# Performance work log

Measured on AMD Instinct MI355X. Metric: run time of the kernel, lower is better.

## Reference

```python
import jax, jax.numpy as jnp
import numpy as np

B, N, D, H, DG = 1, 1024, 512, 8, 64
DK = D // H
EPS = 1e-5


def _layer_norm(x, g, b):
    m = jnp.mean(x, axis=-1, keepdims=True)
    v = jnp.var(x, axis=-1, keepdims=True)
    return (x - m) / jnp.sqrt(v + EPS) * g + b


def _box_rel_embedding(box):
    # box: (B, N, 4) = x_min, y_min, x_max, y_max
    x_min, y_min, x_max, y_max = [box[..., i] for i in range(4)]  # each (B, N)
    cx = (x_min + x_max) * 0.5
    cy = (y_min + y_max) * 0.5
    w = x_max - x_min + 1.0
    h = y_max - y_min + 1.0
    dx = jnp.log(jnp.clip(jnp.abs((cx[:, :, None] - cx[:, None, :]) / w[:, :, None]), 0.001))
    dy = jnp.log(jnp.clip(jnp.abs((cy[:, :, None] - cy[:, None, :]) / h[:, :, None]), 0.001))
    dw = jnp.log(w[:, :, None] / w[:, None, :])
    dh = jnp.log(h[:, :, None] / h[:, None, :])
    pos = jnp.stack([dx, dy, dw, dh], axis=-1)  # (B, N, N, 4)
    dim_mat = 1.0 / jnp.power(1000.0, jnp.arange(DG // 8, dtype=jnp.float32) / (DG // 8))  # (8,)
    mul = (100.0 * pos[..., None] * dim_mat).reshape(pos.shape[0], pos.shape[1], pos.shape[2], -1)  # (B,N,N,32)
    return jnp.concatenate([jnp.sin(mul), jnp.cos(mul)], axis=-1)  # (B, N, N, 64)


def _split_heads(x, W, b):
    # torch permute(2,0,1,3).view(-1, len, d_k): head-major flattening
    return (x @ W.T + b).reshape(B, N, H, DK).transpose(2, 0, 1, 3).reshape(H * B, N, DK)


def _forward(input_query, input_key, input_value, input_box,
             Wq, bq, Wk, bk, Wv, bv, Wo, bo, WG_w, WG_b,
             ln0_g, ln0_b, ln_g, ln_b):
    residual = input_query
    emb = _box_rel_embedding(input_box)  # (B, N, N, 64)
    # per-head linear (64 -> 1) then relu: (B, H, N, N)
    w_g = jax.nn.relu(jnp.einsum('bijg,hg->bhij', emb, WG_w) + WG_b[None, :, None, None])
    q = _split_heads(input_query, Wq, bq)  # (H*B, N, DK)
    k = _split_heads(input_key, Wk, bk)
    v = _split_heads(input_value, Wv, bv)
    scores = jnp.einsum('xnd,xmd->xnm', q, k) / np.sqrt(DK).astype(np.float32)  # (H*B, N, N)
    # original adds (B,H,N,N) to (H*B,N,N): only valid for B==1
    w_mn = jax.nn.softmax(jnp.log(jnp.clip(w_g.reshape(H * B, N, N), 1e-6)) + scores, axis=-1)
    x = jnp.einsum('xnm,xmd->xnd', w_mn, v)  # (H*B, N, DK)
    # faithful to original: transpose(1,2) then view(nbatches, -1, h*d_k)
    x = x.transpose(0, 2, 1).reshape(B, -1, H * DK)  # (B, N, D)
    out0 = _layer_norm(x + residual, ln0_g, ln0_b)
    out = out0 @ Wo.T + bo  # dropout = identity (eval mode)
    return _layer_norm(out + out0, ln_g, ln_b)


def setup_inputs() -> dict:
    key = jax.random.key(0)
    ks = jax.random.split(key, 12)
    inp = {}
    inp['input_query'] = jax.random.normal(ks[0], (B, N, D), dtype=jnp.float32)
    inp['input_key'] = jax.random.normal(ks[1], (B, N, D), dtype=jnp.float32)
    inp['input_value'] = jax.random.normal(ks[2], (B, N, D), dtype=jnp.float32)
    mins = jax.random.uniform(ks[3], (B, N, 2), dtype=jnp.float32) * 500.0
    sizes = jax.random.uniform(ks[4], (B, N, 2), dtype=jnp.float32) * 99.0 + 1.0
    inp['input_box'] = jnp.concatenate([mins, mins + sizes], axis=-1)  # valid boxes
    s = 0.02
    inp['Wq'] = jax.random.normal(ks[5], (D, D), dtype=jnp.float32) * s
    inp['bq'] = jnp.zeros((D,), dtype=jnp.float32)
    inp['Wk'] = jax.random.normal(ks[6], (D, D), dtype=jnp.float32) * s
    inp['bk'] = jnp.zeros((D,), dtype=jnp.float32)
    inp['Wv'] = jax.random.normal(ks[7], (D, D), dtype=jnp.float32) * s
    inp['bv'] = jnp.zeros((D,), dtype=jnp.float32)
    inp['Wo'] = jax.random.normal(ks[8], (D, D), dtype=jnp.float32) * s
    inp['bo'] = jnp.zeros((D,), dtype=jnp.float32)
    inp['WG_w'] = jax.random.normal(ks[9], (H, DG), dtype=jnp.float32) * 0.1
    inp['WG_b'] = jax.random.normal(ks[10], (H,), dtype=jnp.float32) * 0.1
    inp['ln0_g'] = jnp.ones((D,), dtype=jnp.float32)
    inp['ln0_b'] = jnp.zeros((D,), dtype=jnp.float32)
    inp['ln_g'] = jnp.ones((D,), dtype=jnp.float32)
    inp['ln_b'] = jnp.zeros((D,), dtype=jnp.float32)
    return inp


def reference(input_query, input_key, input_value, input_box,
              Wq, bq, Wk, bk, Wv, bv, Wo, bo, WG_w, WG_b,
              ln0_g, ln0_b, ln_g, ln_b):
    return _forward(input_query, input_key, input_value, input_box,
                    Wq, bq, Wk, bk, Wv, bv, Wo, bo, WG_w, WG_b,
                    ln0_g, ln0_b, ln_g, ln_b)
```

## Files before the change

kernel.cpp:

```cpp
#include <hip/hip_runtime.h>
#include <cstddef>

#define NTOK 1024
#define DMODEL 512
#define NHEAD 8
#define DKH 64
#define NSPLIT 8
#define JQ 128

typedef __attribute__((ext_vector_type(4))) float f32x4;
typedef __attribute__((ext_vector_type(8))) __bf16 bf16x8;
typedef __attribute__((ext_vector_type(4))) __bf16 bf16x4;
typedef __attribute__((ext_vector_type(4))) unsigned short u16x4;
typedef __attribute__((ext_vector_type(8))) unsigned short u16x8;
typedef __attribute__((ext_vector_type(4))) _Float16 f16x4;
typedef unsigned short ushort_t;

__device__ __forceinline__ float wave_sum_f(float v){
  #pragma unroll
  for (int m=1; m<64; m<<=1) v += __shfl_xor(v, m, 64);
  return v;
}
__device__ __forceinline__ unsigned short f2bf(float f){
  __bf16 b = (__bf16)f;
  return __builtin_bit_cast(unsigned short, b);
}
__device__ __forceinline__ float bf2f(unsigned short u){
  return (float)__builtin_bit_cast(__bf16, u);
}

__device__ __forceinline__ float fract_hw(float x){
  float r; asm("v_fract_f32 %0, %1" : "=v"(r) : "v"(x)); return r;
}
__device__ __forceinline__ float sin_rev(float rev){
  float f = fract_hw(rev);
  float s; asm("v_sin_f32 %0, %1" : "=v"(s) : "v"(f)); return s;
}
__device__ __forceinline__ float cos_rev(float rev){
  float f = fract_hw(rev);
  float c; asm("v_cos_f32 %0, %1" : "=v"(c) : "v"(f)); return c;
}
__device__ __forceinline__ float log_hw(float x){
  float l; asm("v_log_f32 %0, %1" : "=v"(l) : "v"(x));
  return 0.69314718056f * l;
}
__device__ __forceinline__ float exp_hw(float x){
  float y = x * 1.44269504f;
  float e; asm("v_exp_f32 %0, %1" : "=v"(e) : "v"(y));
  return e;
}

__global__ __launch_bounds__(256) void k_front2(
    const float* __restrict__ box, const float* __restrict__ WGw, const float* __restrict__ WGb,
    _Float16* __restrict__ wg16,
    const float* __restrict__ inq, const float* __restrict__ ink, const float* __restrict__ inv,
    const float* __restrict__ Wq, const float* __restrict__ Wk, const float* __restrict__ Wv,
    const float* __restrict__ Wo,
    const float* __restrict__ bq, const float* __restrict__ bk, const float* __restrict__ bv,
    ushort_t* __restrict__ Qb, ushort_t* __restrict__ Kb, ushort_t* __restrict__ Vt,
    ushort_t* __restrict__ Wob){
  __shared__ __align__(16) char smem[17408];
  const int t = threadIdx.x;
  const int lane = t & 63, w = t >> 6, li = lane & 15, g = lane >> 4;
  if (blockIdx.x >= 1408){
    int off = ((blockIdx.x - 1408)*256 + t)*8;
    float4 a = *(const float4*)(Wo + off);
    float4 b4 = *(const float4*)(Wo + off + 4);
    u16x4 o0, o1;
    o0[0]=f2bf(a.x); o0[1]=f2bf(a.y); o0[2]=f2bf(a.z); o0[3]=f2bf(a.w);
    o1[0]=f2bf(b4.x); o1[1]=f2bf(b4.y); o1[2]=f2bf(b4.z); o1[3]=f2bf(b4.w);
    *(u16x4*)(Wob + off) = o0;
    *(u16x4*)(Wob + off + 4) = o1;
    return;
  }
  if (blockIdx.x >= 1024){
    const int u = blockIdx.x - 1024;
    const int z = u >> 7;
    const int rem = u & 127;
    const int m0 = (rem >> 3)*64;
    const int n0 = (rem & 7)*64;
    const float* A = z==0 ? inq : z==1 ? ink : inv;
    const float* W = z==0 ? Wq : z==1 ? Wk : Wv;
    const float* bias = z==0 ? bq : z==1 ? bk : bv;
    ushort_t* Al = (ushort_t*)smem;
    ushort_t* Wl = (ushort_t*)(smem + 8704);
    const int row = t >> 2, kq = (t & 3)*16;
    const int mrb = (w >> 1)*32;
    const int nrb = (w & 1)*32;
    f32x4 acc[2][2] = {};
    for (int k0 = 0; k0 < DMODEL; k0 += 64){
      {
        const float* ap = A + (size_t)(m0+row)*DMODEL + k0 + kq;
        const float* wp = W + (size_t)(n0+row)*DMODEL + k0 + kq;
        #pragma unroll
        for (int q=0; q<4; q++){
          float4 av = *(const float4*)(ap + q*4);
          float4 wv = *(const float4*)(wp + q*4);
          u16x4 pa, pw;
          pa[0]=f2bf(av.x); pa[1]=f2bf(av.y); pa[2]=f2bf(av.z); pa[3]=f2bf(av.w);
          pw[0]=f2bf(wv.x); pw[1]=f2bf(wv.y); pw[2]=f2bf(wv.z); pw[3]=f2bf(wv.w);
          *(u16x4*)(Al + row*68 + kq + q*4) = pa;
          *(u16x4*)(Wl + row*68 + kq + q*4) = pw;
        }
      }
      __syncthreads();
      #pragma unroll
      for (int kc=0; kc<64; kc+=32){
        const ushort_t* arl = Al + (mrb + li)*68 + kc + g*8;
        const ushort_t* wrl = Wl + (nrb + li)*68 + kc + g*8;
        bf16x8 af0 = *(const bf16x8*)(arl);
        bf16x8 af1 = *(const bf16x8*)(arl + 16*68);
        bf16x8 wf0 = *(const bf16x8*)(wrl);
        bf16x8 wf1 = *(const bf16x8*)(wrl + 16*68);
        if (z < 2){
          acc[0][0] = __builtin_amdgcn_mfma_f32_16x16x32_bf16(wf0, af0, acc[0][0], 0,0,0);
          acc[0][1] = __builtin_amdgcn_mfma_f32_16x16x32_bf16(wf0, af1, acc[0][1], 0,0,0);
          acc[1][0] = __builtin_amdgcn_mfma_f32_16x16x32_bf16(wf1, af0, acc[1][0], 0,0,0);
          acc[1][1] = __builtin_amdgcn_mfma_f32_16x16x32_bf16(wf1, af1, acc[1][1], 0,0,0);
        } else {
          acc[0][0] = __builtin_amdgcn_mfma_f32_16x16x32_bf16(af0, wf0, acc[0][0], 0,0,0);
          acc[0][1] = __builtin_amdgcn_mfma_f32_16x16x32_bf16(af0, wf1, acc[0][1], 0,0,0);
          acc[1][0] = __builtin_amdgcn_mfma_f32_16x16x32_bf16(af1, wf0, acc[1][0], 0,0,0);
          acc[1][1] = __builtin_amdgcn_mfma_f32_16x16x32_bf16(af1, wf1, acc[1][1], 0,0,0);
        }
      }
      __syncthreads();
    }
    if (z < 2){
      ushort_t* C = z ? Kb : Qb;
      #pragma unroll
      for (int nf=0; nf<2; nf++){
        int n = n0 + nrb + nf*16 + g*4;
        float4 b4 = *(const float4*)(bias + n);
        const float* bp = (const float*)&b4;
        #pragma unroll
        for (int mf=0; mf<2; mf++){
          int m = m0 + mrb + mf*16 + li;
          u16x4 o;
          #pragma unroll
          for (int r=0; r<4; r++) o[r] = f2bf(acc[nf][mf][r] + bp[r]);
          *(u16x4*)(C + (size_t)m*DMODEL + n) = o;
        }
      }
    } else {
      #pragma unroll
      for (int mf=0; mf<2; mf++){
        int m = m0 + mrb + mf*16 + g*4;
        #pragma unroll
        for (int nf=0; nf<2; nf++){
          int n = n0 + nrb + nf*16 + li;
          float bn = bias[n];
          u16x4 o;
          #pragma unroll
          for (int r=0; r<4; r++) o[r] = f2bf(acc[mf][nf][r] + bn);
          *(u16x4*)(Vt + (((size_t)(n>>6))<<16) + ((size_t)(n&63)<<10) + m) = o;
        }
      }
    }
    return;
  }
  float* arr = (float*)smem;
  {
  }
  #pragma unroll
  for (int u2=0; u2<4; u2++){
    int idx = u2*256 + t;
    float4 b4 = *(const float4*)(box + idx*4);
    arr[idx]        = (b4.x + b4.z)*0.5f;
    arr[1024+idx]   = (b4.y + b4.w)*0.5f;
    arr[2048+idx]   = log_hw(b4.z - b4.x + 1.0f);
    arr[3072+idx]   = log_hw(b4.w - b4.y + 1.0f);
  }
  const int i = blockIdx.x;
  float4 bi = *(const float4*)(box + i*4);
  float wi = bi.z - bi.x + 1.0f, hi = bi.w - bi.y + 1.0f;
  float Pi = (g==0) ? (bi.x+bi.z)*0.5f : (g==1) ? (bi.y+bi.w)*0.5f
           : (g==2) ? log_hw(wi) : log_hw(hi);
  float Ri = (g==0) ? 1.0f/wi : (g==1) ? 1.0f/hi : 1.0f;
  const bool doLog = (g < 2);
  bf16x8 wfs = {}, wfc = {};
  float wgb_li = 0.0f;
  if (li < 8){
    #pragma unroll
    for (int e=0; e<8; e++){
      wfs[e] = (__bf16)WGw[li*64 + g*8 + e];
      wfc[e] = (__bf16)WGw[li*64 + 32 + g*8 + e];
    }
    wgb_li = WGb[li];
  }
  __syncthreads();
  const float* parr = arr + g*1024;
  const float DMrev[8] = {15.9154943f, 6.7115094f, 2.8302196f, 1.1934938f,
                          0.5032921f, 0.2122365f, 0.08949941f, 0.0377416f};
  const int jbeg = w*256;
  for (int it=0; it<16; ++it){
    int j = jbeg + it*16 + li;
    float diff = (Pi - parr[j])*Ri;
    float lg = log_hw(fmaxf(fabsf(diff), 1e-3f));
    float dv = doLog ? lg : diff;
    bf16x8 afs, afc;
    #pragma unroll
    for (int e=0; e<8; e++){
      float rev = dv * DMrev[e];
      afs[e] = (__bf16)sin_rev(rev);
      afc[e] = (__bf16)cos_rev(rev);
    }
    f32x4 acc = (f32x4){0.f,0.f,0.f,0.f};
    acc = __builtin_amdgcn_mfma_f32_16x16x32_bf16(afs, wfs, acc, 0,0,0);
    acc = __builtin_amdgcn_mfma_f32_16x16x32_bf16(afc, wfc, acc, 0,0,0);
    if (li < 8){
      f16x4 o;
      #pragma unroll
      for (int r=0; r<4; r++)
        o[r] = (_Float16)fmaxf(acc[r] + wgb_li, 6.103515625e-05f);
      *(f16x4*)(wg16 + (((size_t)li<<20) + ((size_t)i<<10) + jbeg + it*16 + g*4)) = o;
    }
  }
}

__global__ __launch_bounds__(512) void k_attn4(const ushort_t* __restrict__ Qb,
     const ushort_t* __restrict__ Kb, const ushort_t* __restrict__ Vt,
     const _Float16* __restrict__ wg, ushort_t* __restrict__ Xpt, float* __restrict__ rsp){
  __shared__ __align__(16) char smem[34816];
  ushort_t* Ks = (ushort_t*)smem;
  ushort_t* Vs = (ushort_t*)(smem + 17408);
  const int t = threadIdx.x;
  const int itg = blockIdx.x, h = blockIdx.y, sp = blockIdx.z;
  const int jbeg = sp*JQ;
  {
    const int r = t >> 3, c = (t & 7)*8;
    #pragma unroll
    for (int p=0; p<2; p++){
      u16x8 kv = *(const u16x8*)(Kb + (size_t)(jbeg + p*64 + r)*DMODEL + h*DKH + c);
      *(u16x8*)(Ks + (p*64 + r)*68 + c) = kv;
      u16x8 vv = *(const u16x8*)(Vt + ((size_t)h<<16) + (size_t)r*NTOK + jbeg + p*64 + c);
      *(u16x8*)(Vs + r*136 + p*64 + c) = vv;
    }
  }
  const int lane = t & 63, w = t >> 6;
  const int i0 = (itg*8 + w)*16;
  const int li = lane & 15, g = lane >> 4;
  const ushort_t* qp = Qb + (size_t)(i0+li)*DMODEL + h*DKH + g*8;
  bf16x8 qf0 = *(const bf16x8*)(qp);
  bf16x8 qf1 = *(const bf16x8*)(qp + 32);
  const _Float16* gbase = wg + ((size_t)h<<20) + ((size_t)(i0+li)<<10) + jbeg + g*4;
  f32x4 xacc[4];
  #pragma unroll
  for (int mf=0; mf<4; mf++) xacc[mf] = (f32x4){0.f,0.f,0.f,0.f};
  float rsum = 0.f;
  __syncthreads();
  #pragma unroll
  for (int jj = 0; jj < JQ; jj += 32){
    const ushort_t* kp = Ks + (jj + li)*68 + g*8;
    bf16x8 a00 = *(const bf16x8*)(kp);
    bf16x8 a01 = *(const bf16x8*)(kp + 32);
    bf16x8 a10 = *(const bf16x8*)(kp + 16*68);
    bf16x8 a11 = *(const bf16x8*)(kp + 16*68 + 32);
    f32x4 s0 = (f32x4){0.f,0.f,0.f,0.f};
    f32x4 s1 = (f32x4){0.f,0.f,0.f,0.f};
    s0 = __builtin_amdgcn_mfma_f32_16x16x32_bf16(a00, qf0, s0, 0,0,0);
    s0 = __builtin_amdgcn_mfma_f32_16x16x32_bf16(a01, qf1, s0, 0,0,0);
    s1 = __builtin_amdgcn_mfma_f32_16x16x32_bf16(a10, qf0, s1, 0,0,0);
    s1 = __builtin_amdgcn_mfma_f32_16x16x32_bf16(a11, qf1, s1, 0,0,0);
    f16x4 g0 = *(const f16x4*)(gbase + jj);
    f16x4 g1 = *(const f16x4*)(gbase + jj + 16);
    float p[8];
    #pragma unroll
    for (int r=0; r<4; r++){ p[r]   = (float)g0[r] * exp_hw(s0[r]*0.125f); rsum += p[r]; }
    #pragma unroll
    for (int r=0; r<4; r++){ p[4+r] = (float)g1[r] * exp_hw(s1[r]*0.125f); rsum += p[4+r]; }
    bf16x8 pb;
    pb[0]=(__bf16)p[0]; pb[1]=(__bf16)p[1]; pb[2]=(__bf16)p[2]; pb[3]=(__bf16)p[3];
    pb[4]=(__bf16)p[4]; pb[5]=(__bf16)p[5]; pb[6]=(__bf16)p[6]; pb[7]=(__bf16)p[7];
    #pragma unroll
    for (int mf=0; mf<4; mf++){
      const ushort_t* vp = Vs + (size_t)(li + mf*16)*136 + jj + g*4;
      bf16x4 lo = *(const bf16x4*)(vp);
      bf16x4 hi = *(const bf16x4*)(vp + 16);
      bf16x8 vf = __builtin_shufflevector(lo, hi, 0,1,2,3,4,5,6,7);
      xacc[mf] = __builtin_amdgcn_mfma_f32_16x16x32_bf16(vf, pb, xacc[mf], 0,0,0);
    }
  }
  rsum += __shfl_xor(rsum, 16, 64);
  rsum += __shfl_xor(rsum, 32, 64);
  if (lane < 16) rsp[((size_t)sp*NHEAD + h)*NTOK + i0 + li] = rsum;
  __syncthreads();
  float* xw = (float*)smem + w*(16*68);
  #pragma unroll
  for (int mf=0; mf<4; mf++)
    *(f32x4*)&xw[li*68 + mf*16 + g*4] = xacc[mf];
  __builtin_amdgcn_s_waitcnt(0);
  float xv[16];
  #pragma unroll
  for (int r=0; r<16; r++) xv[r] = xw[r*68 + lane];
  u16x8 o0, o1;
  #pragma unroll
  for (int r=0; r<8; r++){ o0[r] = f2bf(xv[r]); o1[r] = f2bf(xv[8+r]); }
  ushort_t* xp = Xpt + (((size_t)sp*NHEAD + h)*DKH + lane)*NTOK + i0;
  *(u16x8*)(xp)     = o0;
  *(u16x8*)(xp + 8) = o1;
}

__global__ __launch_bounds__(256) void k_ln0c(const ushort_t* __restrict__ Xpt,
        const float* __restrict__ rsp, const float* __restrict__ resid,
        const float* __restrict__ g, const float* __restrict__ b,
        float* __restrict__ out0, ushort_t* __restrict__ out0b){
  const int n = blockIdx.x, t = threadIdx.x;
  const int h = n >> 7, dk = (n >> 1) & 63, mo = (n & 1)*512;
  const int i0 = mo + t, i1 = mo + t + 256;
  float s0v=0.f, s1v=0.f, r0=0.f, r1=0.f;
  #pragma unroll
  for (int sp=0; sp<NSPLIT; sp++){
    const ushort_t* base = Xpt + (((size_t)sp*NHEAD + h)*DKH + dk)*NTOK;
    s0v += bf2f(base[i0]);
    s1v += bf2f(base[i1]);
    const float* rb = rsp + ((size_t)sp*NHEAD + h)*NTOK;
    r0 += rb[i0];
    r1 += rb[i1];
  }
  float x0 = s0v/r0 + resid[(size_t)n*DMODEL + t];
  float x1 = s1v/r1 + resid[(size_t)n*DMODEL + t + 256];
  __shared__ float red[8];
  float s = wave_sum_f(x0 + x1);
  float q = wave_sum_f(x0*x0 + x1*x1);
  int wid = t >> 6, lane = t & 63;
  if (lane == 0){ red[wid] = s; red[4+wid] = q; }
  __syncthreads();
  float S = red[0]+red[1]+red[2]+red[3];
  float Q = red[4]+red[5]+red[6]+red[7];
  float mean = S * (1.0f/512.0f);
  float var = Q * (1.0f/512.0f) - mean*mean;
  float rs = rsqrtf(var + 1e-5f);
  float y0 = (x0-mean)*rs*g[t] + b[t];
  float y1 = (x1-mean)*rs*g[t+256] + b[t+256];
  out0[(size_t)n*DMODEL + t]        = y0;
  out0[(size_t)n*DMODEL + t + 256]  = y1;
  out0b[(size_t)n*DMODEL + t]       = f2bf(y0);
  out0b[(size_t)n*DMODEL + t + 256] = f2bf(y1);
}

__global__ __launch_bounds__(512) void k_mm_o_ln(
    const ushort_t* __restrict__ A, const ushort_t* __restrict__ W,
    const float* __restrict__ bo, const float* __restrict__ add,
    const float* __restrict__ lng, const float* __restrict__ lnb, float* __restrict__ out){
  const int t = threadIdx.x, lane = t & 63, w = t >> 6;
  const int li = lane & 15, g = lane >> 4;
  const int m0 = blockIdx.x*16;
  const int n0 = w*64;
  const ushort_t* ar = A + (size_t)(m0+li)*DMODEL + g*8;
  const ushort_t* wr = W + (size_t)(n0+li)*DMODEL + g*8;
  f32x4 acc[4] = {};
  #pragma unroll
  for (int k0=0; k0<DMODEL; k0+=64){
    bf16x8 afa = *(const bf16x8*)(ar + k0);
    bf16x8 afb = *(const bf16x8*)(ar + k0 + 32);
    #pragma unroll
    for (int nf=0; nf<4; nf++){
      const ushort_t* wp = wr + (size_t)nf*16*DMODEL + k0;
      bf16x8 wfa = *(const bf16x8*)(wp);
      bf16x8 wfb = *(const bf16x8*)(wp + 32);
      acc[nf] = __builtin_amdgcn_mfma_f32_16x16x32_bf16(wfa, afa, acc[nf], 0,0,0);
      acc[nf] = __builtin_amdgcn_mfma_f32_16x16x32_bf16(wfb, afb, acc[nf], 0,0,0);
    }
  }
  const int m = m0 + li;
  float s = 0.f, qq = 0.f;
  f32x4 v[4];
  #pragma unroll
  for (int nf=0; nf<4; nf++){
    int n = n0 + nf*16 + g*4;
    f32x4 b4 = *(const f32x4*)(bo + n);
    f32x4 a4 = *(const f32x4*)(add + (size_t)m*DMODEL + n);
    #pragma unroll
    for (int r=0; r<4; r++){
      float x = acc[nf][r] + b4[r] + a4[r];
      v[nf][r] = x; s += x; qq += x*x;
    }
  }
  s  += __shfl_xor(s, 16, 64);  s  += __shfl_xor(s, 32, 64);
  qq += __shfl_xor(qq, 16, 64); qq += __shfl_xor(qq, 32, 64);
  __shared__ float red[8][16][2];
  if (g == 0){ red[w][li][0] = s; red[w][li][1] = qq; }
  __syncthreads();
  float S = 0.f, Q = 0.f;
  #pragma unroll
  for (int u=0; u<8; u++){ S += red[u][li][0]; Q += red[u][li][1]; }
  float mean = S * (1.0f/512.0f);
  float var = Q * (1.0f/512.0f) - mean*mean;
  float rs = rsqrtf(var + 1e-5f);
  #pragma unroll
  for (int nf=0; nf<4; nf++){
    int n = n0 + nf*16 + g*4;
    f32x4 g4 = *(const f32x4*)(lng + n);
    f32x4 be = *(const f32x4*)(lnb + n);
    f32x4 o;
    #pragma unroll
    for (int r=0; r<4; r++) o[r] = (v[nf][r]-mean)*rs*g4[r] + be[r];
    *(f32x4*)(out + (size_t)m*DMODEL + n) = o;
  }
}

extern "C" void kernel_launch(void* const* d_in, const int* in_sizes, int n_in,
                              void* d_out, int out_size, void* d_ws, size_t ws_size,
                              hipStream_t stream){
  (void)in_sizes; (void)n_in; (void)out_size; (void)ws_size;
  const float* in_q = (const float*)d_in[0];
  const float* in_k = (const float*)d_in[1];
  const float* in_v = (const float*)d_in[2];
  const float* box  = (const float*)d_in[3];
  const float* Wq   = (const float*)d_in[4];
  const float* bq   = (const float*)d_in[5];
  const float* Wk   = (const float*)d_in[6];
  const float* bk   = (const float*)d_in[7];
  const float* Wv   = (const float*)d_in[8];
  const float* bv   = (const float*)d_in[9];
  const float* Wo   = (const float*)d_in[10];
  const float* bo   = (const float*)d_in[11];
  const float* WGw  = (const float*)d_in[12];
  const float* WGb  = (const float*)d_in[13];
  const float* ln0g = (const float*)d_in[14];
  const float* ln0b = (const float*)d_in[15];
  const float* lng  = (const float*)d_in[16];
  const float* lnb  = (const float*)d_in[17];

  float* ws = (float*)d_ws;
  ushort_t* Wob  = (ushort_t*)(ws + 0);
  ushort_t* Qb   = (ushort_t*)(ws + 131072);
  ushort_t* Kb   = (ushort_t*)(ws + 393216);
  ushort_t* Vt   = (ushort_t*)(ws + 655360);
  _Float16* wg16 = (_Float16*)(ws + 917504);
  ushort_t* Xpt  = (ushort_t*)(ws + 5111808);
  float*    rsp  = ws + 7208960;
  float*    out0 = ws + 7274496;
  ushort_t* out0b= (ushort_t*)(ws + 7798784);
  float*    out  = (float*)d_out;

  k_front2<<<dim3(1536), dim3(256), 0, stream>>>(box, WGw, WGb, wg16,
            in_q, in_k, in_v, Wq, Wk, Wv, Wo, bq, bk, bv, Qb, Kb, Vt, Wob);
  k_attn4<<<dim3(8,8,8), dim3(512), 0, stream>>>(Qb, Kb, Vt, wg16, Xpt, rsp);
  k_ln0c<<<dim3(1024), dim3(256), 0, stream>>>(Xpt, rsp, in_q, ln0g, ln0b, out0, out0b);
  k_mm_o_ln<<<dim3(64), dim3(512), 0, stream>>>(out0b, Wob, bo, out0, lng, lnb, out);
}
```

Measured before the change: 73.26 us.

## Fuse split-combine LayerNorm into output projection kernel and halve attention key splits

Merges the split-K reduction plus first LayerNorm kernel into the Wo matmul plus second LayerNorm kernel. Normalized rows stay in shared memory instead of round-tripping through global memory, and one launch is removed. The attention kernel now uses 4 key splits of 256 instead of 8 of 128, which means fewer partial results to reduce but only half as many blocks (256). The fused back kernel handles 8 rows per block across 128 blocks, so half of each 16-row MFMA tile is wasted.

```diff
diff --git a/kernel.cpp b/kernel.cpp
--- a/kernel.cpp
+++ b/kernel.cpp
@@ -5,8 +5,8 @@
 #define DMODEL 512
 #define NHEAD 8
 #define DKH 64
-#define NSPLIT 8
-#define JQ 128
+#define NSPLIT 4
+#define JQ 256
 
 typedef __attribute__((ext_vector_type(4))) float f32x4;
 typedef __attribute__((ext_vector_type(8))) __bf16 bf16x8;
@@ -160,8 +160,6 @@
     return;
   }
   float* arr = (float*)smem;
-  {
-  }
   #pragma unroll
   for (int u2=0; u2<4; u2++){
     int idx = u2*256 + t;
@@ -218,23 +216,22 @@
   }
 }
 
-__global__ __launch_bounds__(512) void k_attn4(const ushort_t* __restrict__ Qb,
+__global__ __launch_bounds__(512) void k_attn3(const ushort_t* __restrict__ Qb,
      const ushort_t* __restrict__ Kb, const ushort_t* __restrict__ Vt,
      const _Float16* __restrict__ wg, ushort_t* __restrict__ Xpt, float* __restrict__ rsp){
-  __shared__ __align__(16) char smem[34816];
-  ushort_t* Ks = (ushort_t*)smem;
-  ushort_t* Vs = (ushort_t*)(smem + 17408);
+  __shared__ ushort_t Ks[256*68];
+  __shared__ ushort_t Vs[64*264];
   const int t = threadIdx.x;
   const int itg = blockIdx.x, h = blockIdx.y, sp = blockIdx.z;
   const int jbeg = sp*JQ;
   {
     const int r = t >> 3, c = (t & 7)*8;
     #pragma unroll
-    for (int p=0; p<2; p++){
+    for (int p=0; p<4; p++){
       u16x8 kv = *(const u16x8*)(Kb + (size_t)(jbeg + p*64 + r)*DMODEL + h*DKH + c);
       *(u16x8*)(Ks + (p*64 + r)*68 + c) = kv;
       u16x8 vv = *(const u16x8*)(Vt + ((size_t)h<<16) + (size_t)r*NTOK + jbeg + p*64 + c);
-      *(u16x8*)(Vs + r*136 + p*64 + c) = vv;
+      *(u16x8*)(Vs + r*264 + p*64 + c) = vv;
     }
   }
   const int lane = t & 63, w = t >> 6;
@@ -274,7 +271,7 @@
     pb[4]=(__bf16)p[4]; pb[5]=(__bf16)p[5]; pb[6]=(__bf16)p[6]; pb[7]=(__bf16)p[7];
     #pragma unroll
     for (int mf=0; mf<4; mf++){
-      const ushort_t* vp = Vs + (size_t)(li + mf*16)*136 + jj + g*4;
+      const ushort_t* vp = Vs + (size_t)(li + mf*16)*264 + jj + g*4;
       bf16x4 lo = *(const bf16x4*)(vp);
       bf16x4 hi = *(const bf16x4*)(vp + 16);
       bf16x8 vf = __builtin_shufflevector(lo, hi, 0,1,2,3,4,5,6,7);
@@ -285,7 +282,7 @@
   rsum += __shfl_xor(rsum, 32, 64);
   if (lane < 16) rsp[((size_t)sp*NHEAD + h)*NTOK + i0 + li] = rsum;
   __syncthreads();
-  float* xw = (float*)smem + w*(16*68);
+  float* xw = (float*)Ks + w*(16*68);
   #pragma unroll
   for (int mf=0; mf<4; mf++)
     *(f32x4*)&xw[li*68 + mf*16 + g*4] = xacc[mf];
@@ -301,54 +298,54 @@
   *(u16x8*)(xp + 8) = o1;
 }
 
-__global__ __launch_bounds__(256) void k_ln0c(const ushort_t* __restrict__ Xpt,
-        const float* __restrict__ rsp, const float* __restrict__ resid,
-        const float* __restrict__ g, const float* __restrict__ b,
-        float* __restrict__ out0, ushort_t* __restrict__ out0b){
-  const int n = blockIdx.x, t = threadIdx.x;
-  const int h = n >> 7, dk = (n >> 1) & 63, mo = (n & 1)*512;
-  const int i0 = mo + t, i1 = mo + t + 256;
-  float s0v=0.f, s1v=0.f, r0=0.f, r1=0.f;
-  #pragma unroll
-  for (int sp=0; sp<NSPLIT; sp++){
-    const ushort_t* base = Xpt + (((size_t)sp*NHEAD + h)*DKH + dk)*NTOK;
-    s0v += bf2f(base[i0]);
-    s1v += bf2f(base[i1]);
-    const float* rb = rsp + ((size_t)sp*NHEAD + h)*NTOK;
-    r0 += rb[i0];
-    r1 += rb[i1];
-  }
-  float x0 = s0v/r0 + resid[(size_t)n*DMODEL + t];
-  float x1 = s1v/r1 + resid[(size_t)n*DMODEL + t + 256];
-  __shared__ float red[8];
-  float s = wave_sum_f(x0 + x1);
-  float q = wave_sum_f(x0*x0 + x1*x1);
-  int wid = t >> 6, lane = t & 63;
-  if (lane == 0){ red[wid] = s; red[4+wid] = q; }
-  __syncthreads();
-  float S = red[0]+red[1]+red[2]+red[3];
-  float Q = red[4]+red[5]+red[6]+red[7];
-  float mean = S * (1.0f/512.0f);
-  float var = Q * (1.0f/512.0f) - mean*mean;
-  float rs = rsqrtf(var + 1e-5f);
-  float y0 = (x0-mean)*rs*g[t] + b[t];
-  float y1 = (x1-mean)*rs*g[t+256] + b[t+256];
-  out0[(size_t)n*DMODEL + t]        = y0;
-  out0[(size_t)n*DMODEL + t + 256]  = y1;
-  out0b[(size_t)n*DMODEL + t]       = f2bf(y0);
-  out0b[(size_t)n*DMODEL + t + 256] = f2bf(y1);
-}
-
-__global__ __launch_bounds__(512) void k_mm_o_ln(
-    const ushort_t* __restrict__ A, const ushort_t* __restrict__ W,
-    const float* __restrict__ bo, const float* __restrict__ add,
-    const float* __restrict__ lng, const float* __restrict__ lnb, float* __restrict__ out){
+__global__ __launch_bounds__(512) void k_back2(
+    const ushort_t* __restrict__ Xpt, const float* __restrict__ rsp,
+    const float* __restrict__ inq,
+    const float* __restrict__ ln0g, const float* __restrict__ ln0b,
+    const ushort_t* __restrict__ Wob, const float* __restrict__ bo,
+    const float* __restrict__ lng, const float* __restrict__ lnb,
+    float* __restrict__ out){
+  __shared__ ushort_t Ab[8][520];
+  __shared__ float    Y[8][516];
+  __shared__ float    red[8][8][2];
   const int t = threadIdx.x, lane = t & 63, w = t >> 6;
   const int li = lane & 15, g = lane >> 4;
-  const int m0 = blockIdx.x*16;
+  const int m0 = blockIdx.x*8;
+  {
+    const int n = m0 + w;
+    const int h = n >> 7, dk = (n >> 1) & 63, mo = (n & 1)*512;
+    float x[8];
+    float sum = 0.f, sq = 0.f;
+    #pragma unroll
+    for (int c=0; c<8; c++){
+      int d = c*64 + lane;
+      int i = mo + d;
+      float sv = 0.f, rv = 0.f;
+      #pragma unroll
+      for (int sp=0; sp<NSPLIT; sp++){
+        sv += bf2f(Xpt[(((size_t)sp*NHEAD + h)*DKH + dk)*NTOK + i]);
+        rv += rsp[((size_t)sp*NHEAD + h)*NTOK + i];
+      }
+      x[c] = sv/rv + inq[(size_t)n*DMODEL + d];
+      sum += x[c]; sq += x[c]*x[c];
+    }
+    sum = wave_sum_f(sum);
+    sq  = wave_sum_f(sq);
+    float mean = sum * (1.0f/512.0f);
+    float var = sq * (1.0f/512.0f) - mean*mean;
+    float rs = rsqrtf(var + 1e-5f);
+    #pragma unroll
+    for (int c=0; c<8; c++){
+      int d = c*64 + lane;
+      float y = (x[c]-mean)*rs*ln0g[d] + ln0b[d];
+      Y[w][d] = y;
+      Ab[w][d] = f2bf(y);
+    }
+  }
+  __syncthreads();
   const int n0 = w*64;
-  const ushort_t* ar = A + (size_t)(m0+li)*DMODEL + g*8;
-  const ushort_t* wr = W + (size_t)(n0+li)*DMODEL + g*8;
+  const ushort_t* ar = &Ab[li & 7][g*8];
+  const ushort_t* wr = Wob + (size_t)(n0+li)*DMODEL + g*8;
   f32x4 acc[4] = {};
   #pragma unroll
   for (int k0=0; k0<DMODEL; k0+=64){
@@ -363,40 +360,40 @@
       acc[nf] = __builtin_amdgcn_mfma_f32_16x16x32_bf16(wfb, afb, acc[nf], 0,0,0);
     }
   }
-  const int m = m0 + li;
   float s = 0.f, qq = 0.f;
   f32x4 v[4];
   #pragma unroll
   for (int nf=0; nf<4; nf++){
     int n = n0 + nf*16 + g*4;
     f32x4 b4 = *(const f32x4*)(bo + n);
-    f32x4 a4 = *(const f32x4*)(add + (size_t)m*DMODEL + n);
     #pragma unroll
     for (int r=0; r<4; r++){
-      float x = acc[nf][r] + b4[r] + a4[r];
+      float x = acc[nf][r] + b4[r] + Y[li & 7][n + r];
       v[nf][r] = x; s += x; qq += x*x;
     }
   }
   s  += __shfl_xor(s, 16, 64);  s  += __shfl_xor(s, 32, 64);
   qq += __shfl_xor(qq, 16, 64); qq += __shfl_xor(qq, 32, 64);
-  __shared__ float red[8][16][2];
-  if (g == 0){ red[w][li][0] = s; red[w][li][1] = qq; }
+  if (g == 0 && li < 8){ red[w][li][0] = s; red[w][li][1] = qq; }
   __syncthreads();
   float S = 0.f, Q = 0.f;
   #pragma unroll
-  for (int u=0; u<8; u++){ S += red[u][li][0]; Q += red[u][li][1]; }
+  for (int u=0; u<8; u++){ S += red[u][li & 7][0]; Q += red[u][li & 7][1]; }
   float mean = S * (1.0f/512.0f);
   float var = Q * (1.0f/512.0f) - mean*mean;
   float rs = rsqrtf(var + 1e-5f);
-  #pragma unroll
-  for (int nf=0; nf<4; nf++){
-    int n = n0 + nf*16 + g*4;
-    f32x4 g4 = *(const f32x4*)(lng + n);
-    f32x4 be = *(const f32x4*)(lnb + n);
-    f32x4 o;
-    #pragma unroll
-    for (int r=0; r<4; r++) o[r] = (v[nf][r]-mean)*rs*g4[r] + be[r];
-    *(f32x4*)(out + (size_t)m*DMODEL + n) = o;
+  if (li < 8){
+    const int m = m0 + li;
+    #pragma unroll
+    for (int nf=0; nf<4; nf++){
+      int n = n0 + nf*16 + g*4;
+      f32x4 g4 = *(const f32x4*)(lng + n);
+      f32x4 be = *(const f32x4*)(lnb + n);
+      f32x4 o;
+      #pragma unroll
+      for (int r=0; r<4; r++) o[r] = (v[nf][r]-mean)*rs*g4[r] + be[r];
+      *(f32x4*)(out + (size_t)m*DMODEL + n) = o;
+    }
   }
 }
 
@@ -430,14 +427,12 @@
   ushort_t* Vt   = (ushort_t*)(ws + 655360);
   _Float16* wg16 = (_Float16*)(ws + 917504);
   ushort_t* Xpt  = (ushort_t*)(ws + 5111808);
-  float*    rsp  = ws + 7208960;
-  float*    out0 = ws + 7274496;
-  ushort_t* out0b= (ushort_t*)(ws + 7798784);
+  float*    rsp  = ws + 6160384;
   float*    out  = (float*)d_out;
 
   k_front2<<<dim3(1536), dim3(256), 0, stream>>>(box, WGw, WGb, wg16,
             in_q, in_k, in_v, Wq, Wk, Wv, Wo, bq, bk, bv, Qb, Kb, Vt, Wob);
-  k_attn4<<<dim3(8,8,8), dim3(512), 0, stream>>>(Qb, Kb, Vt, wg16, Xpt, rsp);
-  k_ln0c<<<dim3(1024), dim3(256), 0, stream>>>(Xpt, rsp, in_q, ln0g, ln0b, out0, out0b);
-  k_mm_o_ln<<<dim3(64), dim3(512), 0, stream>>>(out0b, Wob, bo, out0, lng, lnb, out);
-}
+  k_attn3<<<dim3(8,8,4), dim3(512), 0, stream>>>(Qb, Kb, Vt, wg16, Xpt, rsp);
+  k_back2<<<dim3(128), dim3(512), 0, stream>>>(Xpt, rsp, in_q, ln0g, ln0b,
+            Wob, bo, lng, lnb, out);
+}
```

After: 66.73 us, median of 2. 8.9% less time.
